# Performance work log

Measured on AMD Instinct MI355X. Metric: run time of the kernel, lower is better.

The kernel has to match this reference:

```python
import jax, jax.numpy as jnp
import numpy as np

TOP_K = 8


def setup_inputs() -> dict:
    key = jax.random.key(0)
    k1, k2 = jax.random.split(key)
    B, S, D, E = 4, 4096, 2048, 64
    x = jax.random.normal(k1, (B, S, D), dtype=jnp.float32)
    # nn.Linear(d_model, n_experts): weight [E, D], bias [E]
    W = jax.random.normal(k2, (E, D), dtype=jnp.float32) * (1.0 / np.sqrt(D))
    b = jnp.zeros((E,), dtype=jnp.float32)
    return {"x": x, "W": W, "b": b}


def reference(x, W, b):
    # logits: [B, S, E] = x @ W^T + b
    logits = jnp.einsum("bsd,ed->bse", x, W) + b
    scores = jax.nn.sigmoid(logits)                      # [B, S, E]
    B, S, E = scores.shape
    flat = scores.reshape(B * S, E)                      # tokens x experts
    top_w, top_idx = jax.lax.top_k(flat, TOP_K)          # [B*S, k]
    return top_w.reshape(B, S, TOP_K), top_idx.reshape(B, S, TOP_K)
```

## Files before the change

### kernel.cpp

```cpp
#include <hip/hip_runtime.h>
#include <math.h>

#define TOKENS 16384
#define DMODEL 2048
#define NEXP   64
#define TOPK   8
#define WSHORTS 12288

typedef unsigned short u16;
typedef float f32x4 __attribute__((ext_vector_type(4)));
typedef short s16x8 __attribute__((ext_vector_type(8)));

__device__ __forceinline__ u16 f2bf(float f, float& back) {
    unsigned u = __float_as_uint(f);
    unsigned r = u + 0x7fffu + ((u >> 16) & 1u);
    back = __uint_as_float(r & 0xffff0000u);
    return (u16)(r >> 16);
}

__global__ __launch_bounds__(256) void wconv(
    const float* __restrict__ W, u16* __restrict__ wimg)
{
    const int id  = blockIdx.x * 256 + threadIdx.x;
    const int e   = id >> 8;
    const int ko8 = id & 255;
    const int k0  = ko8 * 8;
    const int c   = ko8 >> 3;
    const int ks  = (ko8 >> 2) & 1;
    const int hi  = ko8 & 3;
    const int lane = hi * 16 + (e & 15);
    const int eq   = e >> 4;

    const float* src = W + (size_t)e * DMODEL + k0;
    const float4 f0 = *(const float4*)(src);
    const float4 f1 = *(const float4*)(src + 4);
    const float xe[8] = {f0.x, f0.y, f0.z, f0.w, f1.x, f1.y, f1.z, f1.w};
    s16x8 va, vb, vc;
#pragma unroll
    for (int j = 0; j < 8; ++j) {
        float b1, b2, b3;
        const u16 a1 = f2bf(xe[j], b1);
        const float d1 = xe[j] - b1;
        const u16 a2 = f2bf(d1, b2);
        const float d2 = d1 - b2;
        const u16 a3 = f2bf(d2, b3);
        va[j] = (short)a1; vb[j] = (short)a2; vc[j] = (short)a3;
    }
    u16* base = wimg + (size_t)c * WSHORTS + lane * 8;
    *(s16x8*)(base + ((0 * 2 + ks) * 4 + eq) * 512) = va;
    *(s16x8*)(base + ((1 * 2 + ks) * 4 + eq) * 512) = vb;
    *(s16x8*)(base + ((2 * 2 + ks) * 4 + eq) * 512) = vc;
}

__global__ __launch_bounds__(256, 4) void router_fused(
    const float* __restrict__ x, const u16* __restrict__ wimg,
    const float* __restrict__ bias, float* __restrict__ out_w,
    float* __restrict__ out_i)
{
    __shared__ double lg[2][16][NEXP];

    const int tid  = threadIdx.x;
    const int lane = tid & 63;
    const int w    = tid >> 6;
    const int eh   = w & 1;
    const int kh   = w >> 1;
    const size_t tokBase = (size_t)blockIdx.x * 16;

    const int arow = lane & 15;
    const float* xrow = x + (tokBase + arow) * (size_t)DMODEL + kh * 1024 +
                        (lane >> 4) * 8;
    const u16* wt0 = wimg + (size_t)kh * 16 * WSHORTS +
                     (size_t)(eh * 2) * 512 + lane * 8;

    f32x4  acc[2][2];
    double accd[2][4];
#pragma unroll
    for (int i = 0; i < 2; ++i)
#pragma unroll
        for (int j = 0; j < 2; ++j) acc[i][j] = (f32x4){0.f, 0.f, 0.f, 0.f};
#pragma unroll
    for (int j = 0; j < 2; ++j)
#pragma unroll
        for (int r = 0; r < 4; ++r) accd[j][r] = 0.0;

    float4 xv[4];
    xv[0] = *(const float4*)(xrow);
    xv[1] = *(const float4*)(xrow + 4);
    xv[2] = *(const float4*)(xrow + 32);
    xv[3] = *(const float4*)(xrow + 36);

    for (int t = 0; t < 16; ++t) {
        const u16* wt = wt0 + (size_t)t * WSHORTS;
        s16x8 b[3][2][2];
#pragma unroll
        for (int tau = 0; tau < 3; ++tau)
#pragma unroll
            for (int ks = 0; ks < 2; ++ks)
#pragma unroll
                for (int nt = 0; nt < 2; ++nt)
                    b[tau][ks][nt] = *(const s16x8*)(
                        wt + ((tau * 2 + ks) * 4 + nt) * 512);

        s16x8 af[3][2];
#pragma unroll
        for (int ks = 0; ks < 2; ++ks) {
            const float xe[8] = {xv[ks * 2].x,     xv[ks * 2].y,
                                 xv[ks * 2].z,     xv[ks * 2].w,
                                 xv[ks * 2 + 1].x, xv[ks * 2 + 1].y,
                                 xv[ks * 2 + 1].z, xv[ks * 2 + 1].w};
#pragma unroll
            for (int j = 0; j < 8; ++j) {
                float b1, b2, b3;
                const u16 a1 = f2bf(xe[j], b1);
                const float d1 = xe[j] - b1;
                const u16 a2 = f2bf(d1, b2);
                const float d2 = d1 - b2;
                const u16 a3 = f2bf(d2, b3);
                af[0][ks][j] = (short)a1;
                af[1][ks][j] = (short)a2;
                af[2][ks][j] = (short)a3;
            }
        }
        if (t + 1 < 16) {
            const float* xp = xrow + (size_t)(t + 1) * 64;
            xv[0] = *(const float4*)(xp);
            xv[1] = *(const float4*)(xp + 4);
            xv[2] = *(const float4*)(xp + 32);
            xv[3] = *(const float4*)(xp + 36);
        }
#pragma unroll
        for (int ks = 0; ks < 2; ++ks)
#pragma unroll
            for (int nt = 0; nt < 2; ++nt) {
                f32x4 t0 = acc[ks][nt];
                t0 = __builtin_amdgcn_mfma_f32_16x16x32_bf16(af[0][ks], b[0][ks][nt], t0, 0, 0, 0);
                t0 = __builtin_amdgcn_mfma_f32_16x16x32_bf16(af[0][ks], b[1][ks][nt], t0, 0, 0, 0);
                t0 = __builtin_amdgcn_mfma_f32_16x16x32_bf16(af[1][ks], b[0][ks][nt], t0, 0, 0, 0);
                t0 = __builtin_amdgcn_mfma_f32_16x16x32_bf16(af[0][ks], b[2][ks][nt], t0, 0, 0, 0);
                t0 = __builtin_amdgcn_mfma_f32_16x16x32_bf16(af[2][ks], b[0][ks][nt], t0, 0, 0, 0);
                t0 = __builtin_amdgcn_mfma_f32_16x16x32_bf16(af[1][ks], b[1][ks][nt], t0, 0, 0, 0);
                acc[ks][nt] = t0;
            }
#pragma unroll
        for (int nt = 0; nt < 2; ++nt)
#pragma unroll
            for (int r = 0; r < 4; ++r) {
                accd[nt][r] += (double)acc[0][nt][r] + (double)acc[1][nt][r];
                acc[0][nt][r] = 0.f;
                acc[1][nt][r] = 0.f;
            }
    }

#pragma unroll
    for (int nt = 0; nt < 2; ++nt)
#pragma unroll
        for (int r = 0; r < 4; ++r) {
            const int row = (lane >> 4) * 4 + r;
            const int col = eh * 32 + nt * 16 + (lane & 15);
            lg[kh][row][col] = accd[nt][r];
        }
    __syncthreads();

    const float be = bias[lane];
#pragma unroll
    for (int i = 0; i < 4; ++i) {
        const int tl = w * 4 + i;
        float v = (float)(lg[0][tl][lane] + lg[1][tl][lane]) + be;
        const int myi = lane;
        float bv = 0.0f; int bi = 0;
#pragma unroll
        for (int r = 0; r < TOPK; ++r) {
            float mv = v; int mi = myi;
#pragma unroll
            for (int off = 32; off > 0; off >>= 1) {
                const float ov = __shfl_xor(mv, off, 64);
                const int   oi = __shfl_xor(mi, off, 64);
                if (ov > mv || (ov == mv && oi < mi)) { mv = ov; mi = oi; }
            }
            if (lane == r) { bv = mv; bi = mi; }
            if (myi == mi) { v = -INFINITY; }
        }
        if (lane < TOPK) {
            const size_t tok = tokBase + tl;
            out_w[tok * TOPK + lane] = 1.0f / (1.0f + expf(-bv));
            out_i[tok * TOPK + lane] = (float)bi;
        }
    }
}

extern "C" void kernel_launch(void* const* d_in, const int* in_sizes, int n_in,
                              void* d_out, int out_size, void* d_ws, size_t ws_size,
                              hipStream_t stream) {
    const float* x    = (const float*)d_in[0];
    const float* W    = (const float*)d_in[1];
    const float* bias = (const float*)d_in[2];
    float* out_w = (float*)d_out;
    float* out_i = (float*)d_out + (size_t)TOKENS * TOPK;
    u16* wimg = (u16*)d_ws;

    wconv<<<dim3((NEXP * DMODEL / 8) / 256), 256, 0, stream>>>(W, wimg);
    router_fused<<<dim3(TOKENS / 16), 256, 0, stream>>>(x, wimg, bias, out_w, out_i);
}
```

Measured before the change: 253.6 us.

## Process 32 tokens per block to reuse weight fragments across two token tiles

```diff
diff --git a/kernel.cpp b/kernel.cpp
--- a/kernel.cpp
+++ b/kernel.cpp
@@ -52,42 +52,46 @@
     *(s16x8*)(base + ((2 * 2 + ks) * 4 + eq) * 512) = vc;
 }
 
-__global__ __launch_bounds__(256, 4) void router_fused(
+__global__ __launch_bounds__(256) void router_fused(
     const float* __restrict__ x, const u16* __restrict__ wimg,
     const float* __restrict__ bias, float* __restrict__ out_w,
     float* __restrict__ out_i)
 {
-    __shared__ double lg[2][16][NEXP];
+    __shared__ double lg[2][32][NEXP];
 
     const int tid  = threadIdx.x;
     const int lane = tid & 63;
     const int w    = tid >> 6;
     const int eh   = w & 1;
     const int kh   = w >> 1;
-    const size_t tokBase = (size_t)blockIdx.x * 16;
+    const size_t tokBase = (size_t)blockIdx.x * 32;
 
     const int arow = lane & 15;
-    const float* xrow = x + (tokBase + arow) * (size_t)DMODEL + kh * 1024 +
-                        (lane >> 4) * 8;
+    const float* xrow0 = x + (tokBase + arow) * (size_t)DMODEL + kh * 1024 +
+                         (lane >> 4) * 8;
+    const float* xrow1 = xrow0 + (size_t)16 * DMODEL;
     const u16* wt0 = wimg + (size_t)kh * 16 * WSHORTS +
                      (size_t)(eh * 2) * 512 + lane * 8;
 
-    f32x4  acc[2][2];
-    double accd[2][4];
+    f32x4  acc0[2][2], acc1[2][2];
+    double accd0[2][4], accd1[2][4];
 #pragma unroll
     for (int i = 0; i < 2; ++i)
 #pragma unroll
-        for (int j = 0; j < 2; ++j) acc[i][j] = (f32x4){0.f, 0.f, 0.f, 0.f};
+        for (int j = 0; j < 2; ++j) {
+            acc0[i][j] = (f32x4){0.f, 0.f, 0.f, 0.f};
+            acc1[i][j] = (f32x4){0.f, 0.f, 0.f, 0.f};
+        }
 #pragma unroll
     for (int j = 0; j < 2; ++j)
 #pragma unroll
-        for (int r = 0; r < 4; ++r) accd[j][r] = 0.0;
-
-    float4 xv[4];
-    xv[0] = *(const float4*)(xrow);
-    xv[1] = *(const float4*)(xrow + 4);
-    xv[2] = *(const float4*)(xrow + 32);
-    xv[3] = *(const float4*)(xrow + 36);
+        for (int r = 0; r < 4; ++r) { accd0[j][r] = 0.0; accd1[j][r] = 0.0; }
+
+    float4 xv0[4], xv1[4];
+    xv0[0] = *(const float4*)(xrow0);      xv0[1] = *(const float4*)(xrow0 + 4);
+    xv0[2] = *(const float4*)(xrow0 + 32); xv0[3] = *(const float4*)(xrow0 + 36);
+    xv1[0] = *(const float4*)(xrow1);      xv1[1] = *(const float4*)(xrow1 + 4);
+    xv1[2] = *(const float4*)(xrow1 + 32); xv1[3] = *(const float4*)(xrow1 + 36);
 
     for (int t = 0; t < 16; ++t) {
         const u16* wt = wt0 + (size_t)t * WSHORTS;
@@ -104,10 +108,10 @@
         s16x8 af[3][2];
 #pragma unroll
         for (int ks = 0; ks < 2; ++ks) {
-            const float xe[8] = {xv[ks * 2].x,     xv[ks * 2].y,
-                                 xv[ks * 2].z,     xv[ks * 2].w,
-                                 xv[ks * 2 + 1].x, xv[ks * 2 + 1].y,
-                                 xv[ks * 2 + 1].z, xv[ks * 2 + 1].w};
+            const float xe[8] = {xv0[ks * 2].x,     xv0[ks * 2].y,
+                                 xv0[ks * 2].z,     xv0[ks * 2].w,
+                                 xv0[ks * 2 + 1].x, xv0[ks * 2 + 1].y,
+                                 xv0[ks * 2 + 1].z, xv0[ks * 2 + 1].w};
 #pragma unroll
             for (int j = 0; j < 8; ++j) {
                 float b1, b2, b3;
@@ -122,32 +126,72 @@
             }
         }
         if (t + 1 < 16) {
-            const float* xp = xrow + (size_t)(t + 1) * 64;
-            xv[0] = *(const float4*)(xp);
-            xv[1] = *(const float4*)(xp + 4);
-            xv[2] = *(const float4*)(xp + 32);
-            xv[3] = *(const float4*)(xp + 36);
+            const float* xp = xrow0 + (size_t)(t + 1) * 64;
+            xv0[0] = *(const float4*)(xp);      xv0[1] = *(const float4*)(xp + 4);
+            xv0[2] = *(const float4*)(xp + 32); xv0[3] = *(const float4*)(xp + 36);
         }
 #pragma unroll
         for (int ks = 0; ks < 2; ++ks)
 #pragma unroll
             for (int nt = 0; nt < 2; ++nt) {
-                f32x4 t0 = acc[ks][nt];
+                f32x4 t0 = acc0[ks][nt];
                 t0 = __builtin_amdgcn_mfma_f32_16x16x32_bf16(af[0][ks], b[0][ks][nt], t0, 0, 0, 0);
                 t0 = __builtin_amdgcn_mfma_f32_16x16x32_bf16(af[0][ks], b[1][ks][nt], t0, 0, 0, 0);
                 t0 = __builtin_amdgcn_mfma_f32_16x16x32_bf16(af[1][ks], b[0][ks][nt], t0, 0, 0, 0);
                 t0 = __builtin_amdgcn_mfma_f32_16x16x32_bf16(af[0][ks], b[2][ks][nt], t0, 0, 0, 0);
                 t0 = __builtin_amdgcn_mfma_f32_16x16x32_bf16(af[2][ks], b[0][ks][nt], t0, 0, 0, 0);
                 t0 = __builtin_amdgcn_mfma_f32_16x16x32_bf16(af[1][ks], b[1][ks][nt], t0, 0, 0, 0);
-                acc[ks][nt] = t0;
-            }
+                acc0[ks][nt] = t0;
+            }
+
+#pragma unroll
+        for (int ks = 0; ks < 2; ++ks) {
+            const float xe[8] = {xv1[ks * 2].x,     xv1[ks * 2].y,
+                                 xv1[ks * 2].z,     xv1[ks * 2].w,
+                                 xv1[ks * 2 + 1].x, xv1[ks * 2 + 1].y,
+                                 xv1[ks * 2 + 1].z, xv1[ks * 2 + 1].w};
+#pragma unroll
+            for (int j = 0; j < 8; ++j) {
+                float b1, b2, b3;
+                const u16 a1 = f2bf(xe[j], b1);
+                const float d1 = xe[j] - b1;
+                const u16 a2 = f2bf(d1, b2);
+                const float d2 = d1 - b2;
+                const u16 a3 = f2bf(d2, b3);
+                af[0][ks][j] = (short)a1;
+                af[1][ks][j] = (short)a2;
+                af[2][ks][j] = (short)a3;
+            }
+        }
+        if (t + 1 < 16) {
+            const float* xp = xrow1 + (size_t)(t + 1) * 64;
+            xv1[0] = *(const float4*)(xp);      xv1[1] = *(const float4*)(xp + 4);
+            xv1[2] = *(const float4*)(xp + 32); xv1[3] = *(const float4*)(xp + 36);
+        }
+#pragma unroll
+        for (int ks = 0; ks < 2; ++ks)
+#pragma unroll
+            for (int nt = 0; nt < 2; ++nt) {
+                f32x4 t0 = acc1[ks][nt];
+                t0 = __builtin_amdgcn_mfma_f32_16x16x32_bf16(af[0][ks], b[0][ks][nt], t0, 0, 0, 0);
+                t0 = __builtin_amdgcn_mfma_f32_16x16x32_bf16(af[0][ks], b[1][ks][nt], t0, 0, 0, 0);
+                t0 = __builtin_amdgcn_mfma_f32_16x16x32_bf16(af[1][ks], b[0][ks][nt], t0, 0, 0, 0);
+                t0 = __builtin_amdgcn_mfma_f32_16x16x32_bf16(af[0][ks], b[2][ks][nt], t0, 0, 0, 0);
+                t0 = __builtin_amdgcn_mfma_f32_16x16x32_bf16(af[2][ks], b[0][ks][nt], t0, 0, 0, 0);
+                t0 = __builtin_amdgcn_mfma_f32_16x16x32_bf16(af[1][ks], b[1][ks][nt], t0, 0, 0, 0);
+                acc1[ks][nt] = t0;
+            }
+
 #pragma unroll
         for (int nt = 0; nt < 2; ++nt)
 #pragma unroll
             for (int r = 0; r < 4; ++r) {
-                accd[nt][r] += (double)acc[0][nt][r] + (double)acc[1][nt][r];
-                acc[0][nt][r] = 0.f;
-                acc[1][nt][r] = 0.f;
+                accd0[nt][r] += (double)acc0[0][nt][r] + (double)acc0[1][nt][r];
+                acc0[0][nt][r] = 0.f;
+                acc0[1][nt][r] = 0.f;
+                accd1[nt][r] += (double)acc1[0][nt][r] + (double)acc1[1][nt][r];
+                acc1[0][nt][r] = 0.f;
+                acc1[1][nt][r] = 0.f;
             }
     }
 
@@ -157,14 +201,15 @@
         for (int r = 0; r < 4; ++r) {
             const int row = (lane >> 4) * 4 + r;
             const int col = eh * 32 + nt * 16 + (lane & 15);
-            lg[kh][row][col] = accd[nt][r];
+            lg[kh][row][col]      = accd0[nt][r];
+            lg[kh][row + 16][col] = accd1[nt][r];
         }
     __syncthreads();
 
     const float be = bias[lane];
 #pragma unroll
-    for (int i = 0; i < 4; ++i) {
-        const int tl = w * 4 + i;
+    for (int i = 0; i < 8; ++i) {
+        const int tl = w * 8 + i;
         float v = (float)(lg[0][tl][lane] + lg[1][tl][lane]) + be;
         const int myi = lane;
         float bv = 0.0f; int bi = 0;
@@ -199,5 +244,5 @@
     u16* wimg = (u16*)d_ws;
 
     wconv<<<dim3((NEXP * DMODEL / 8) / 256), 256, 0, stream>>>(W, wimg);
-    router_fused<<<dim3(TOKENS / 16), 256, 0, stream>>>(x, wimg, bias, out_w, out_i);
-}
+    router_fused<<<dim3(TOKENS / 32), 256, 0, stream>>>(x, wimg, bias, out_w, out_i);
+}
```

Measured after the change: 256.4 us. No clear change (+1.1%).

## Split-K router GEMM with LDS-staged weights and separate reduce/top-k kernel

Applied to the files above, without the earlier changes.

```diff
diff --git a/kernel.cpp b/kernel.cpp
--- a/kernel.cpp
+++ b/kernel.cpp
@@ -6,6 +6,7 @@
 #define NEXP   64
 #define TOPK   8
 #define WSHORTS 12288
+#define KSPLIT  16
 
 typedef unsigned short u16;
 typedef float f32x4 __attribute__((ext_vector_type(4)));
@@ -52,139 +53,122 @@
     *(s16x8*)(base + ((2 * 2 + ks) * 4 + eq) * 512) = vc;
 }
 
-__global__ __launch_bounds__(256, 4) void router_fused(
+__global__ __launch_bounds__(512) void router_mfma(
     const float* __restrict__ x, const u16* __restrict__ wimg,
-    const float* __restrict__ bias, float* __restrict__ out_w,
-    float* __restrict__ out_i)
+    float* __restrict__ part)
 {
-    __shared__ double lg[2][16][NEXP];
+    __shared__ __align__(16) u16 Bls[2 * WSHORTS];
 
     const int tid  = threadIdx.x;
     const int lane = tid & 63;
     const int w    = tid >> 6;
-    const int eh   = w & 1;
-    const int kh   = w >> 1;
-    const size_t tokBase = (size_t)blockIdx.x * 16;
+    const int ksp  = blockIdx.y;
+    const size_t tokBase = (size_t)blockIdx.x * 512;
 
-    const int arow = lane & 15;
-    const float* xrow = x + (tokBase + arow) * (size_t)DMODEL + kh * 1024 +
-                        (lane >> 4) * 8;
-    const u16* wt0 = wimg + (size_t)kh * 16 * WSHORTS +
-                     (size_t)(eh * 2) * 512 + lane * 8;
+    {
+        const float4* src = (const float4*)(wimg + (size_t)ksp * 2 * WSHORTS);
+        float4* dst = (float4*)Bls;
+#pragma unroll
+        for (int r = 0; r < 6; ++r)
+            dst[r * 512 + tid] = src[r * 512 + tid];
+    }
+    __syncthreads();
 
-    f32x4  acc[2][2];
-    double accd[2][4];
+    const int hi = lane >> 4;
+    const float* xw = x + (tokBase + (size_t)w * 64 + (lane & 15)) * DMODEL +
+                      ksp * 128 + hi * 8;
+
+#pragma unroll 1
+    for (int tg = 0; tg < 4; ++tg) {
+        double accd[4][4];
 #pragma unroll
-    for (int i = 0; i < 2; ++i)
+        for (int nt = 0; nt < 4; ++nt)
 #pragma unroll
-        for (int j = 0; j < 2; ++j) acc[i][j] = (f32x4){0.f, 0.f, 0.f, 0.f};
+            for (int r = 0; r < 4; ++r) accd[nt][r] = 0.0;
+
+        for (int kc = 0; kc < 4; ++kc) {
+            const float* xp = xw + (size_t)tg * 16 * DMODEL + kc * 32;
+            const float4 a0 = *(const float4*)(xp);
+            const float4 a1 = *(const float4*)(xp + 4);
+
+            s16x8 af0, af1, af2;
+            {
+                const float xe[8] = {a0.x, a0.y, a0.z, a0.w,
+                                     a1.x, a1.y, a1.z, a1.w};
 #pragma unroll
-    for (int j = 0; j < 2; ++j)
+                for (int j = 0; j < 8; ++j) {
+                    float b1, b2, b3;
+                    const u16 t1 = f2bf(xe[j], b1);
+                    const float d1 = xe[j] - b1;
+                    const u16 t2 = f2bf(d1, b2);
+                    const float d2 = d1 - b2;
+                    const u16 t3 = f2bf(d2, b3);
+                    af0[j] = (short)t1; af1[j] = (short)t2; af2[j] = (short)t3;
+                }
+            }
+
+            const u16* bb = Bls + (size_t)(kc >> 1) * WSHORTS +
+                            (kc & 1) * 2048 + lane * 8;
+
 #pragma unroll
-        for (int r = 0; r < 4; ++r) accd[j][r] = 0.0;
-
-    float4 xv[4];
-    xv[0] = *(const float4*)(xrow);
-    xv[1] = *(const float4*)(xrow + 4);
-    xv[2] = *(const float4*)(xrow + 32);
-    xv[3] = *(const float4*)(xrow + 36);
-
-    for (int t = 0; t < 16; ++t) {
-        const u16* wt = wt0 + (size_t)t * WSHORTS;
-        s16x8 b[3][2][2];
+            for (int nt = 0; nt < 4; ++nt) {
+                const s16x8 b1 = *(const s16x8*)(bb + 0 * 4096 + nt * 512);
+                const s16x8 b2 = *(const s16x8*)(bb + 1 * 4096 + nt * 512);
+                const s16x8 b3 = *(const s16x8*)(bb + 2 * 4096 + nt * 512);
+                f32x4 t0 = (f32x4){0.f, 0.f, 0.f, 0.f};
+                t0 = __builtin_amdgcn_mfma_f32_16x16x32_bf16(af0, b1, t0, 0, 0, 0);
+                t0 = __builtin_amdgcn_mfma_f32_16x16x32_bf16(af0, b2, t0, 0, 0, 0);
+                t0 = __builtin_amdgcn_mfma_f32_16x16x32_bf16(af1, b1, t0, 0, 0, 0);
+                t0 = __builtin_amdgcn_mfma_f32_16x16x32_bf16(af0, b3, t0, 0, 0, 0);
+                t0 = __builtin_amdgcn_mfma_f32_16x16x32_bf16(af2, b1, t0, 0, 0, 0);
+                t0 = __builtin_amdgcn_mfma_f32_16x16x32_bf16(af1, b2, t0, 0, 0, 0);
 #pragma unroll
-        for (int tau = 0; tau < 3; ++tau)
-#pragma unroll
-            for (int ks = 0; ks < 2; ++ks)
-#pragma unroll
-                for (int nt = 0; nt < 2; ++nt)
-                    b[tau][ks][nt] = *(const s16x8*)(
-                        wt + ((tau * 2 + ks) * 4 + nt) * 512);
-
-        s16x8 af[3][2];
-#pragma unroll
-        for (int ks = 0; ks < 2; ++ks) {
-            const float xe[8] = {xv[ks * 2].x,     xv[ks * 2].y,
-                                 xv[ks * 2].z,     xv[ks * 2].w,
-                                 xv[ks * 2 + 1].x, xv[ks * 2 + 1].y,
-                                 xv[ks * 2 + 1].z, xv[ks * 2 + 1].w};
-#pragma unroll
-            for (int j = 0; j < 8; ++j) {
-                float b1, b2, b3;
-                const u16 a1 = f2bf(xe[j], b1);
-                const float d1 = xe[j] - b1;
-                const u16 a2 = f2bf(d1, b2);
-                const float d2 = d1 - b2;
-                const u16 a3 = f2bf(d2, b3);
-                af[0][ks][j] = (short)a1;
-                af[1][ks][j] = (short)a2;
-                af[2][ks][j] = (short)a3;
+                for (int r = 0; r < 4; ++r) accd[nt][r] += (double)t0[r];
             }
         }
-        if (t + 1 < 16) {
-            const float* xp = xrow + (size_t)(t + 1) * 64;
-            xv[0] = *(const float4*)(xp);
-            xv[1] = *(const float4*)(xp + 4);
-            xv[2] = *(const float4*)(xp + 32);
-            xv[3] = *(const float4*)(xp + 36);
-        }
+
 #pragma unroll
-        for (int ks = 0; ks < 2; ++ks)
-#pragma unroll
-            for (int nt = 0; nt < 2; ++nt) {
-                f32x4 t0 = acc[ks][nt];
-                t0 = __builtin_amdgcn_mfma_f32_16x16x32_bf16(af[0][ks], b[0][ks][nt], t0, 0, 0, 0);
-                t0 = __builtin_amdgcn_mfma_f32_16x16x32_bf16(af[0][ks], b[1][ks][nt], t0, 0, 0, 0);
-                t0 = __builtin_amdgcn_mfma_f32_16x16x32_bf16(af[1][ks], b[0][ks][nt], t0, 0, 0, 0);
-                t0 = __builtin_amdgcn_mfma_f32_16x16x32_bf16(af[0][ks], b[2][ks][nt], t0, 0, 0, 0);
-                t0 = __builtin_amdgcn_mfma_f32_16x16x32_bf16(af[2][ks], b[0][ks][nt], t0, 0, 0, 0);
-                t0 = __builtin_amdgcn_mfma_f32_16x16x32_bf16(af[1][ks], b[1][ks][nt], t0, 0, 0, 0);
-                acc[ks][nt] = t0;
-            }
-#pragma unroll
-        for (int nt = 0; nt < 2; ++nt)
+        for (int nt = 0; nt < 4; ++nt)
 #pragma unroll
             for (int r = 0; r < 4; ++r) {
-                accd[nt][r] += (double)acc[0][nt][r] + (double)acc[1][nt][r];
-                acc[0][nt][r] = 0.f;
-                acc[1][nt][r] = 0.f;
+                const size_t tok = tokBase + w * 64 + tg * 16 + hi * 4 + r;
+                part[((size_t)ksp * TOKENS + tok) * NEXP + nt * 16 +
+                     (lane & 15)] = (float)accd[nt][r];
             }
     }
+}
 
+__global__ __launch_bounds__(256) void router_reduce_topk(
+    const float* __restrict__ part, const float* __restrict__ bias,
+    float* __restrict__ out_w, float* __restrict__ out_i, int ksplit)
+{
+    const int lane = threadIdx.x & 63;
+    const int wid  = threadIdx.x >> 6;
+    const size_t t = (size_t)blockIdx.x * 4 + wid;
+
+    double vd = (double)bias[lane];
+    for (int kc = 0; kc < ksplit; ++kc)
+        vd += (double)part[((size_t)kc * TOKENS + t) * NEXP + lane];
+    float v = (float)vd;
+
+    const int myi = lane;
+    float bv = 0.0f; int bi = 0;
 #pragma unroll
-    for (int nt = 0; nt < 2; ++nt)
+    for (int r = 0; r < TOPK; ++r) {
+        float mv = v; int mi = myi;
 #pragma unroll
-        for (int r = 0; r < 4; ++r) {
-            const int row = (lane >> 4) * 4 + r;
-            const int col = eh * 32 + nt * 16 + (lane & 15);
-            lg[kh][row][col] = accd[nt][r];
+        for (int off = 32; off > 0; off >>= 1) {
+            const float ov = __shfl_xor(mv, off, 64);
+            const int   oi = __shfl_xor(mi, off, 64);
+            if (ov > mv || (ov == mv && oi < mi)) { mv = ov; mi = oi; }
         }
-    __syncthreads();
+        if (lane == r)  { bv = mv; bi = mi; }
+        if (myi == mi)  { v = -INFINITY; }
+    }
 
-    const float be = bias[lane];
-#pragma unroll
-    for (int i = 0; i < 4; ++i) {
-        const int tl = w * 4 + i;
-        float v = (float)(lg[0][tl][lane] + lg[1][tl][lane]) + be;
-        const int myi = lane;
-        float bv = 0.0f; int bi = 0;
-#pragma unroll
-        for (int r = 0; r < TOPK; ++r) {
-            float mv = v; int mi = myi;
-#pragma unroll
-            for (int off = 32; off > 0; off >>= 1) {
-                const float ov = __shfl_xor(mv, off, 64);
-                const int   oi = __shfl_xor(mi, off, 64);
-                if (ov > mv || (ov == mv && oi < mi)) { mv = ov; mi = oi; }
-            }
-            if (lane == r) { bv = mv; bi = mi; }
-            if (myi == mi) { v = -INFINITY; }
-        }
-        if (lane < TOPK) {
-            const size_t tok = tokBase + tl;
-            out_w[tok * TOPK + lane] = 1.0f / (1.0f + expf(-bv));
-            out_i[tok * TOPK + lane] = (float)bi;
-        }
+    if (lane < TOPK) {
+        out_w[t * TOPK + lane] = 1.0f / (1.0f + expf(-bv));
+        out_i[t * TOPK + lane] = (float)bi;
     }
 }
 
@@ -196,8 +180,11 @@
     const float* bias = (const float*)d_in[2];
     float* out_w = (float*)d_out;
     float* out_i = (float*)d_out + (size_t)TOKENS * TOPK;
-    u16* wimg = (u16*)d_ws;
+    u16*   wimg = (u16*)d_ws;
+    float* part = (float*)((char*)d_ws + (1 << 20));
 
     wconv<<<dim3((NEXP * DMODEL / 8) / 256), 256, 0, stream>>>(W, wimg);
-    router_fused<<<dim3(TOKENS / 16), 256, 0, stream>>>(x, wimg, bias, out_w, out_i);
+    router_mfma<<<dim3(TOKENS / 512, KSPLIT), 512, 0, stream>>>(x, wimg, part);
+    router_reduce_topk<<<TOKENS / 4, 256, 0, stream>>>(part, bias, out_w, out_i,
+                                                       KSPLIT);
 }
```

Result: no change. 250.8 us (-1.1%).
